# Optimization experiments

Hardware: AMD Instinct MI355X
Metric: run time of the kernel (lower is better)

## Reference

```python
import jax, jax.numpy as jnp
import numpy as np

B, S, D, V = 512, 64, 128, 256
NH = 4                 # sLSTM heads
HD = D // NH           # 32
INNER = 2 * D          # mLSTM inner dim (proj_factor=2.0)
NHM = 4                # mLSTM heads
DHM = INNER // NHM     # 64
BS = 4                 # qkv_proj_blocksize
NB = INNER // BS       # 64 block-diagonal qkv blocks
K = 4                  # causal conv kernel
FF = D                 # gated FFN up dim (proj_factor=1.0)


def setup_inputs():
    key = jax.random.key(0)
    ks = iter(jax.random.split(key, 40))
    def rn(shape, scale=0.02):
        return jax.random.normal(next(ks), shape, dtype=jnp.float32) * scale
    return {
        "x": jax.random.randint(next(ks), (B, S), 0, V, dtype=jnp.int32),
        "embed": rn((V, D), 0.02),
        "s_ln1": jnp.ones((2, D), jnp.float32),
        "s_gates_w": rn((2, 4, NH, HD, HD), 0.08),   # i,f,z,o headwise input projections
        "s_rec": rn((2, 4, NH, HD, HD), 0.08),       # block-diagonal recurrent kernels
        "s_bias": rn((2, 4, NH, HD), 0.1),
        "s_gn": jnp.ones((2, D), jnp.float32),
        "s_ln2": jnp.ones((2, D), jnp.float32),
        "s_ff_up": rn((2, D, 2 * FF), 0.05),
        "s_ff_down": rn((2, FF, D), 0.05),
        "m_ln1": jnp.ones((2, D), jnp.float32),
        "m_up": rn((2, D, 2 * INNER), 0.05),
        "m_conv_w": rn((2, INNER, K), 0.1),
        "m_conv_b": jnp.zeros((2, INNER), jnp.float32),
        "m_qkv_w": rn((2, 3, NB, BS, BS), 0.2),
        "m_ig_w": rn((2, 3 * INNER, NHM), 0.02),
        "m_ig_b": jnp.zeros((2, NHM), jnp.float32),
        "m_fg_w": rn((2, 3 * INNER, NHM), 0.02),
        "m_fg_b": 3.0 * jnp.ones((2, NHM), jnp.float32),
        "m_skip": jnp.ones((2, INNER), jnp.float32),
        "m_onorm": jnp.ones((2, INNER), jnp.float32),
        "m_down": rn((2, INNER, D), 0.05),
        "m_ln2": jnp.ones((2, D), jnp.float32),
        "m_ff_up": rn((2, D, 2 * FF), 0.05),
        "m_ff_down": rn((2, FF, D), 0.05),
        "post_ln": jnp.ones((D,), jnp.float32),
        "head_w": rn((D, V), 0.05),
        "head_b": jnp.zeros((V,), jnp.float32),
    }


def _ln(x, w, eps=1e-5):
    mu = x.mean(-1, keepdims=True)
    var = x.var(-1, keepdims=True)
    return (x - mu) * jax.lax.rsqrt(var + eps) * w


def _mh_ln(xh, w, eps=1e-5):
    # xh: [B,S,nh,dh]; per-head layernorm (GroupNorm), weight-only affine
    mu = xh.mean(-1, keepdims=True)
    var = xh.var(-1, keepdims=True)
    y = (xh - mu) * jax.lax.rsqrt(var + eps)
    return y * w.reshape(xh.shape[-2], xh.shape[-1])


def _ffn(x, up, down):
    g, u = jnp.split(x @ up, 2, axis=-1)
    return (jax.nn.gelu(g) * u) @ down


def _slstm(x, gw, rw, bias, gn):
    # vanilla sLSTM: stabilized exp-gated scalar-memory recurrence, block-diag recurrent kernels
    Bq, Sq, Dq = x.shape
    xh = x.reshape(Bq, Sq, NH, HD)
    # precompute input contributions for all 4 gates: [S,B,4,NH,HD]
    gx = jnp.einsum('bsnd,gned->sbgne', xh, gw) + bias

    def step(carry, g):
        h, c, n, m = carry
        raw = g + jnp.einsum('bnd,gned->bgne', h, rw)
        i_r, f_r, z_r, o_r = raw[:, 0], raw[:, 1], raw[:, 2], raw[:, 3]
        logfplusm = m + jax.nn.log_sigmoid(f_r)
        m_new = jnp.maximum(i_r, logfplusm)
        i = jnp.exp(i_r - m_new)
        f = jnp.exp(logfplusm - m_new)
        c_new = f * c + i * jnp.tanh(z_r)
        n_new = f * n + i
        h_new = jax.nn.sigmoid(o_r) * c_new / n_new
        return (h_new, c_new, n_new, m_new), h_new

    z0 = jnp.zeros((Bq, NH, HD), x.dtype)
    _, ys = jax.lax.scan(step, (z0, z0, z0, z0), gx)
    y = jnp.transpose(ys, (1, 0, 2, 3))  # [B,S,NH,HD]
    return _mh_ln(y, gn).reshape(Bq, Sq, Dq)


def _mlstm(x, up, cw, cb, qkvw, igw, igb, fgw, fgb, skip, onw, down):
    # pre-up-projection mLSTM layer with parallel stabilized matrix-memory cell
    Bq, Sq, _ = x.shape
    xm, z = jnp.split(x @ up, 2, axis=-1)  # [B,S,INNER] each
    # causal depthwise conv + swish
    conv = jax.lax.conv_general_dilated(
        xm.transpose(0, 2, 1), cw[:, None, :],
        window_strides=(1,), padding=[(K - 1, 0)], feature_group_count=INNER)
    x_conv = jax.nn.silu(conv.transpose(0, 2, 1) + cb)

    def hw(t, w):  # block-diagonal (headwise) linear, w: [NB, out, in]
        th = t.reshape(Bq, Sq, NB, BS)
        return jnp.einsum('bsni,noi->bsno', th, w).reshape(Bq, Sq, INNER)

    q = hw(x_conv, qkvw[0])
    k = hw(x_conv, qkvw[1])
    v = hw(xm, qkvw[2])

    gate_in = jnp.concatenate([q, k, v], axis=-1)          # [B,S,3*INNER]
    ig = (gate_in @ igw + igb).transpose(0, 2, 1)          # [B,NHM,S]
    fg = (gate_in @ fgw + fgb).transpose(0, 2, 1)

    qh = q.reshape(Bq, Sq, NHM, DHM).transpose(0, 2, 1, 3)  # [B,NHM,S,DHM]
    kh = k.reshape(Bq, Sq, NHM, DHM).transpose(0, 2, 1, 3)
    vh = v.reshape(Bq, Sq, NHM, DHM).transpose(0, 2, 1, 3)

    log_f = jax.nn.log_sigmoid(fg)                          # [B,NHM,S]
    c = jnp.concatenate([jnp.zeros_like(log_f[..., :1]), jnp.cumsum(log_f, -1)], -1)
    mat = c[..., 1:, None] - c[..., None, 1:]               # (i,j): sum_{t=j+1..i} log f_t
    mask = jnp.tril(jnp.ones((Sq, Sq), bool))
    log_D = jnp.where(mask, mat, -jnp.inf) + ig[..., None, :]
    max_log_D = jnp.max(log_D, -1, keepdims=True)           # [B,NHM,S,1]
    Dm = jnp.exp(log_D - max_log_D)
    qk = jnp.einsum('bhid,bhjd->bhij', qh, kh) * (DHM ** -0.5)
    Cm = qk * Dm
    norm = jnp.maximum(jnp.abs(Cm.sum(-1, keepdims=True)), jnp.exp(-max_log_D))
    Cn = Cm / (norm + 1e-6)
    h = jnp.einsum('bhij,bhjd->bhid', Cn, vh).transpose(0, 2, 1, 3)  # [B,S,NHM,DHM]
    h = _mh_ln(h, onw).reshape(Bq, Sq, INNER)
    h = (h + skip * x_conv) * jax.nn.silu(z)
    return h @ down


def _forward(x, embed, s_ln1, s_gates_w, s_rec, s_bias, s_gn, s_ln2, s_ff_up, s_ff_down,
             m_ln1, m_up, m_conv_w, m_conv_b, m_qkv_w, m_ig_w, m_ig_b, m_fg_w, m_fg_b,
             m_skip, m_onorm, m_down, m_ln2, m_ff_up, m_ff_down, post_ln, head_w, head_b):
    h = embed[x]  # [B,S,D]
    for i in range(2):
        # sLSTM block (even positions 0, 2)
        h = h + _slstm(_ln(h, s_ln1[i]), s_gates_w[i], s_rec[i], s_bias[i], s_gn[i])
        h = h + _ffn(_ln(h, s_ln2[i]), s_ff_up[i], s_ff_down[i])
        # mLSTM block (odd positions 1, 3)
        h = h + _mlstm(_ln(h, m_ln1[i]), m_up[i], m_conv_w[i], m_conv_b[i], m_qkv_w[i],
                       m_ig_w[i], m_ig_b[i], m_fg_w[i], m_fg_b[i], m_skip[i], m_onorm[i], m_down[i])
        h = h + _ffn(_ln(h, m_ln2[i]), m_ff_up[i], m_ff_down[i])
    h = _ln(h, post_ln)
    return h @ head_w + head_b


def reference(x, embed, s_ln1, s_gates_w, s_rec, s_bias, s_gn, s_ln2, s_ff_up, s_ff_down,
              m_ln1, m_up, m_conv_w, m_conv_b, m_qkv_w, m_ig_w, m_ig_b, m_fg_w, m_fg_b,
              m_skip, m_onorm, m_down, m_ln2, m_ff_up, m_ff_down, post_ln, head_w, head_b):
    return _forward(x, embed, s_ln1, s_gates_w, s_rec, s_bias, s_gn, s_ln2, s_ff_up, s_ff_down,
                    m_ln1, m_up, m_conv_w, m_conv_b, m_qkv_w, m_ig_w, m_ig_b, m_fg_w, m_fg_b,
                    m_skip, m_onorm, m_down, m_ln2, m_ff_up, m_ff_down, post_ln, head_w, head_b)
```

## Files before the change

kernel.cpp:

```cpp
#include <hip/hip_runtime.h>
#include <math.h>


__device__ __forceinline__ float sigf(float x){ return 1.f/(1.f+__expf(-x)); }
__device__ __forceinline__ float siluf(float x){ return x/(1.f+__expf(-x)); }
__device__ __forceinline__ float logsigf(float x){ return fminf(x,0.f) - log1pf(__expf(-fabsf(x))); }
__device__ __forceinline__ float geluf(float x){
  return 0.5f*x*(1.f+tanhf(0.7978845608028654f*(x+0.044715f*x*x*x)));
}
__device__ __forceinline__ void sums4(float4 v, float& s, float& q){
  s += v.x+v.y+v.z+v.w;
  q += v.x*v.x+v.y*v.y+v.z*v.z+v.w*v.w;
}

__device__ __forceinline__ void ln_rows(const float* __restrict__ src, const float* __restrict__ lnw,
                                        float* __restrict__ dst, int dstride,
                                        float (*red)[8], float (*red2)[8], int t)
{
  int r = t >> 3, l8 = t & 7;
  const float4* s4 = (const float4*)(src + (size_t)r*128 + l8*16);
  float4 v0=s4[0], v1=s4[1], v2=s4[2], v3=s4[3];
  float su=0.f, sq=0.f;
  sums4(v0,su,sq); sums4(v1,su,sq); sums4(v2,su,sq); sums4(v3,su,sq);
  red[r][l8]=su; red2[r][l8]=sq;
  __syncthreads();
  float ts=0.f, tq=0.f;
  #pragma unroll
  for (int k=0;k<8;k++){ ts+=red[r][k]; tq+=red2[r][k]; }
  float mu = ts*(1.f/128.f);
  float var = tq*(1.f/128.f) - mu*mu;
  float iv = rsqrtf(var+1e-5f);
  int c0 = l8*16;
  float vv[16];
  *(float4*)&vv[0]=v0; *(float4*)&vv[4]=v1; *(float4*)&vv[8]=v2; *(float4*)&vv[12]=v3;
  #pragma unroll
  for (int q2=0;q2<16;q2++) dst[r*dstride + c0 + q2] = (vv[q2]-mu)*iv*lnw[c0+q2];
}

__global__ __launch_bounds__(256) void k_embed(const int* __restrict__ x, const float* __restrict__ embed,
                                               float* __restrict__ h)
{
  int idx4 = blockIdx.x*256 + threadIdx.x;
  int tok = idx4 >> 5;
  int c4  = idx4 & 31;
  int id = x[tok];
  reinterpret_cast<float4*>(h)[idx4] = reinterpret_cast<const float4*>(embed)[id*32 + c4];
}

__global__ __launch_bounds__(512) void k_prep(
    const float* __restrict__ qkvw,
    const float* __restrict__ igw,
    const float* __restrict__ fgw,
    float* __restrict__ wtab)
{
  int t = threadIdx.x;
  int l = t >> 8, c = t & 255;
  int nb = c >> 2, i = c & 3;
  const float* qk  = qkvw + l*3072;
  const float* igl = igw + l*3072;
  const float* fgl = fgw + l*3072;
  float igc[4]={0,0,0,0}, igm[4]={0,0,0,0}, fgc[4]={0,0,0,0}, fgm[4]={0,0,0,0};
  #pragma unroll
  for (int o=0;o<4;o++){
    float wq = qk[nb*16 + o*4 + i];
    float wk = qk[1024 + nb*16 + o*4 + i];
    float wv = qk[2048 + nb*16 + o*4 + i];
    int no = nb*4+o;
    #pragma unroll
    for (int m=0;m<4;m++){
      igc[m] += wq*igl[no*4+m] + wk*igl[(256+no)*4+m];
      igm[m] += wv*igl[(512+no)*4+m];
      fgc[m] += wq*fgl[no*4+m] + wk*fgl[(256+no)*4+m];
      fgm[m] += wv*fgl[(512+no)*4+m];
    }
  }
  float* dst = wtab + l*4096;
  #pragma unroll
  for (int m=0;m<4;m++){
    dst[(0*256+c)*4+m] = igc[m];
    dst[(1*256+c)*4+m] = igm[m];
    dst[(2*256+c)*4+m] = fgc[m];
    dst[(3*256+c)*4+m] = fgm[m];
  }
}

__global__ __launch_bounds__(512) void k_slstm(
    float* __restrict__ h, const float* __restrict__ lnw,
    const float* __restrict__ gw, const float* __restrict__ rw,
    const float* __restrict__ bias, const float* __restrict__ gn)
{
  __shared__ float xh[64][128];
  __shared__ float hb[128];
  __shared__ float raw[512];
  __shared__ float red[64][8];
  __shared__ float red2[64][8];
  __shared__ float mu_s[64][4];
  __shared__ float iv_s[64][4];

  int t = threadIdx.x;
  int b = blockIdx.x;
  float* hrow = h + (size_t)b*8192;

  ln_rows(hrow, lnw, &xh[0][0], 128, red, red2, t);
  __syncthreads();

  int g  = t >> 7;
  int nh = (t >> 5) & 3;
  int e  = t & 31;
  float wg[32], wr[32];
  {
    const float4* g4 = (const float4*)(gw + (((g*4+nh)*32+e)*32));
    const float4* r4 = (const float4*)(rw + (((g*4+nh)*32+e)*32));
    #pragma unroll
    for (int q=0;q<8;q++){
      float4 a=g4[q]; wg[4*q]=a.x; wg[4*q+1]=a.y; wg[4*q+2]=a.z; wg[4*q+3]=a.w;
      float4 c=r4[q]; wr[4*q]=c.x; wr[4*q+1]=c.y; wr[4*q+2]=c.z; wr[4*q+3]=c.w;
    }
  }
  float bs = bias[(g*4+nh)*32+e];
  float c_s=0.f, n_s=0.f, m_s=0.f;
  if (t<128) hb[t]=0.f;
  __syncthreads();

  for (int s=0;s<64;s++){
    const float4* xr = (const float4*)&xh[s][nh*32];
    const float4* hr = (const float4*)&hb[nh*32];
    float acc = bs;
    #pragma unroll
    for (int q=0;q<8;q++){
      float4 xv = xr[q]; float4 hv = hr[q];
      acc += xv.x*wg[4*q+0] + xv.y*wg[4*q+1] + xv.z*wg[4*q+2] + xv.w*wg[4*q+3];
      acc += hv.x*wr[4*q+0] + hv.y*wr[4*q+1] + hv.z*wr[4*q+2] + hv.w*wr[4*q+3];
    }
    raw[t] = acc;
    __syncthreads();
    if (t < 128){
      float i_r = raw[t], f_r = raw[128+t], z_r = raw[256+t], o_r = raw[384+t];
      float lf = m_s + logsigf(f_r);
      float mn = fmaxf(i_r, lf);
      float iv = __expf(i_r-mn), fv = __expf(lf-mn);
      c_s = fv*c_s + iv*tanhf(z_r);
      n_s = fv*n_s + iv;
      m_s = mn;
      float hn = sigf(o_r)*c_s/n_s;
      hb[t] = hn;
      xh[s][t] = hn;
    }
    __syncthreads();
  }

  if (t < 256){
    int s = t>>2, n = t&3;
    const float4* yr = (const float4*)&xh[s][n*32];
    float su=0.f, sq=0.f;
    #pragma unroll
    for (int q=0;q<8;q++){ float4 v = yr[q]; sums4(v,su,sq); }
    float mu = su*(1.f/32.f);
    float var = sq*(1.f/32.f) - mu*mu;
    mu_s[s][n]=mu; iv_s[s][n]=rsqrtf(var+1e-5f);
  }
  __syncthreads();
  #pragma unroll
  for (int rr=0; rr<16; rr++){
    int idx = t + 512*rr;
    int s = idx>>7, c = idx&127;
    float y = (xh[s][c] - mu_s[s][c>>5]) * iv_s[s][c>>5] * gn[c];
    hrow[idx] += y;
  }
}

__global__ __launch_bounds__(256) void k_ffn(
    float* __restrict__ h, const float* __restrict__ lnw,
    const float* __restrict__ up, const float* __restrict__ down)
{
  __shared__ float xln[32][132];
  __shared__ float hid[32][132];
  __shared__ float bws[2][16][256];
  __shared__ float red[32][8];
  __shared__ float red2[32][8];
  int t = threadIdx.x;
  size_t tok0 = (size_t)blockIdx.x * 32;

  ln_rows(h + tok0*128, lnw, &xln[0][0], 132, red, red2, t);
  __syncthreads();

  int r0 = (t >> 5) * 4;
  int c0 = (t & 31) * 4;

  {
    float4 regs[4];
    auto stage = [&](int kc){
      #pragma unroll
      for (int j=0;j<4;j++){
        int idx = t + 256*j;
        int row = idx >> 6, c4 = idx & 63;
        regs[j] = *(const float4*)(up + (size_t)(kc*16+row)*256 + c4*4);
      }
    };
    auto wrt = [&](int buf){
      #pragma unroll
      for (int j=0;j<4;j++){
        int idx = t + 256*j;
        int row = idx >> 6, c4 = idx & 63;
        *(float4*)&bws[buf][row][c4*4] = regs[j];
      }
    };
    stage(0); wrt(0);
    __syncthreads();
    float4 ag[4], au[4];
    #pragma unroll
    for (int i=0;i<4;i++){ ag[i]=make_float4(0,0,0,0); au[i]=make_float4(0,0,0,0); }
    for (int kc=0;kc<8;kc++){
      if (kc<7) stage(kc+1);
      int buf = kc & 1;
      #pragma unroll
      for (int k=0;k<16;k++){
        float4 wg = *(float4*)&bws[buf][k][c0];
        float4 wu = *(float4*)&bws[buf][k][c0+128];
        int kk = kc*16 + k;
        #pragma unroll
        for (int i=0;i<4;i++){
          float xv = xln[r0+i][kk];
          ag[i].x+=xv*wg.x; ag[i].y+=xv*wg.y; ag[i].z+=xv*wg.z; ag[i].w+=xv*wg.w;
          au[i].x+=xv*wu.x; au[i].y+=xv*wu.y; au[i].z+=xv*wu.z; au[i].w+=xv*wu.w;
        }
      }
      if (kc<7) wrt(buf^1);
      __syncthreads();
    }
    #pragma unroll
    for (int i=0;i<4;i++){
      hid[r0+i][c0+0] = geluf(ag[i].x)*au[i].x;
      hid[r0+i][c0+1] = geluf(ag[i].y)*au[i].y;
      hid[r0+i][c0+2] = geluf(ag[i].z)*au[i].z;
      hid[r0+i][c0+3] = geluf(ag[i].w)*au[i].w;
    }
  }
  __syncthreads();

  {
    float (*bw2)[16][128] = (float (*)[16][128])bws;
    float4 regs[2];
    auto stage = [&](int kc){
      #pragma unroll
      for (int j=0;j<2;j++){
        int idx = t + 256*j;
        int row = idx >> 5, c4 = idx & 31;
        regs[j] = *(const float4*)(down + (size_t)(kc*16+row)*128 + c4*4);
      }
    };
    auto wrt = [&](int buf){
      #pragma unroll
      for (int j=0;j<2;j++){
        int idx = t + 256*j;
        int row = idx >> 5, c4 = idx & 31;
        *(float4*)&bw2[buf][row][c4*4] = regs[j];
      }
    };
    stage(0); wrt(0);
    __syncthreads();
    float4 a2[4];
    #pragma unroll
    for (int i=0;i<4;i++) a2[i]=make_float4(0,0,0,0);
    for (int kc=0;kc<8;kc++){
      if (kc<7) stage(kc+1);
      int buf = kc & 1;
      #pragma unroll
      for (int k=0;k<16;k++){
        float4 wv = *(float4*)&bw2[buf][k][c0];
        int kk = kc*16 + k;
        #pragma unroll
        for (int i=0;i<4;i++){
          float xv = hid[r0+i][kk];
          a2[i].x+=xv*wv.x; a2[i].y+=xv*wv.y; a2[i].z+=xv*wv.z; a2[i].w+=xv*wv.w;
        }
      }
      if (kc<7) wrt(buf^1);
      __syncthreads();
    }
    #pragma unroll
    for (int i=0;i<4;i++){
      float* dstp = h + (tok0 + r0 + i)*128 + c0;
      float4 hv = *(float4*)dstp;
      hv.x += a2[i].x; hv.y += a2[i].y; hv.z += a2[i].z; hv.w += a2[i].w;
      *(float4*)dstp = hv;
    }
  }
}

__global__ __launch_bounds__(256) void k_up(
    const float* __restrict__ h, const float* __restrict__ lnw,
    const float* __restrict__ up, float* __restrict__ xm, float* __restrict__ z)
{
  __shared__ float xln[64][132];
  __shared__ float bw[2][32][128];
  __shared__ float red[64][4];
  __shared__ float red2[64][4];
  int t = threadIdx.x;
  int mt = blockIdx.x >> 2, nt = blockIdx.x & 3;
  size_t tok0 = (size_t)mt * 64;
  int n0 = nt * 128;

  {
    int r = t >> 2, l = t & 3;
    const float4* s4 = (const float4*)(h + (tok0 + (size_t)r)*128 + l*32);
    float4 v[8];
    float su=0.f, sq=0.f;
    #pragma unroll
    for (int q=0;q<8;q++){ v[q]=s4[q]; sums4(v[q],su,sq); }
    red[r][l]=su; red2[r][l]=sq;
    __syncthreads();
    float ts=red[r][0]+red[r][1]+red[r][2]+red[r][3];
    float tq=red2[r][0]+red2[r][1]+red2[r][2]+red2[r][3];
    float mu=ts*(1.f/128.f);
    float var=tq*(1.f/128.f)-mu*mu;
    float iv=rsqrtf(var+1e-5f);
    int cb=l*32;
    #pragma unroll
    for (int q=0;q<8;q++){
      xln[r][cb+q*4+0]=(v[q].x-mu)*iv*lnw[cb+q*4+0];
      xln[r][cb+q*4+1]=(v[q].y-mu)*iv*lnw[cb+q*4+1];
      xln[r][cb+q*4+2]=(v[q].z-mu)*iv*lnw[cb+q*4+2];
      xln[r][cb+q*4+3]=(v[q].w-mu)*iv*lnw[cb+q*4+3];
    }
  }

  float4 regs[4];
  auto stage = [&](int kc){
    #pragma unroll
    for (int j=0;j<4;j++){
      int idx = t + 256*j;
      int row = idx >> 5, c4 = idx & 31;
      regs[j] = *(const float4*)(up + (size_t)(kc*32+row)*512 + n0 + c4*4);
    }
  };
  auto wrt = [&](int buf){
    #pragma unroll
    for (int j=0;j<4;j++){
      int idx = t + 256*j;
      int row = idx >> 5, c4 = idx & 31;
      *(float4*)&bw[buf][row][c4*4] = regs[j];
    }
  };
  stage(0); wrt(0);
  __syncthreads();

  int r0 = (t >> 5) * 8;
  int c0 = (t & 31) * 4;
  float4 acc4[8];
  #pragma unroll
  for (int i=0;i<8;i++) acc4[i]=make_float4(0,0,0,0);

  for (int kc=0;kc<4;kc++){
    if (kc<3) stage(kc+1);
    int buf = kc & 1;
    #pragma unroll 8
    for (int k=0;k<32;k++){
      float4 wv = *(float4*)&bw[buf][k][c0];
      int kk = kc*32 + k;
      #pragma unroll
      for (int i=0;i<8;i++){
        float xv = xln[r0+i][kk];
        acc4[i].x += xv*wv.x; acc4[i].y += xv*wv.y; acc4[i].z += xv*wv.z; acc4[i].w += xv*wv.w;
      }
    }
    if (kc<3) wrt(buf^1);
    __syncthreads();
  }

  float* dst; int cbase;
  if (n0 < 256){ dst = xm; cbase = n0 + c0; }
  else         { dst = z;  cbase = n0 - 256 + c0; }
  #pragma unroll
  for (int i=0;i<8;i++)
    *(float4*)(dst + (tok0 + r0 + i)*256 + cbase) = acc4[i];
}

__global__ __launch_bounds__(256) void k_convgates(
    const float* __restrict__ xm, float* __restrict__ xc,
    const float* __restrict__ cw, const float* __restrict__ cb,
    const float* __restrict__ wtab,
    const float* __restrict__ igb, const float* __restrict__ fgb,
    float* __restrict__ ig, float* __restrict__ fg)
{
  int t = threadIdx.x;
  int b = blockIdx.x;
  int c4 = t & 63, sr = t >> 6;
  int c0 = c4*4;
  const float* src = xm + (size_t)b*16384;
  float* dstc = xc + (size_t)b*16384;

  float4 r0 = *(const float4*)(cw + (c0+0)*4);
  float4 r1 = *(const float4*)(cw + (c0+1)*4);
  float4 r2 = *(const float4*)(cw + (c0+2)*4);
  float4 r3 = *(const float4*)(cw + (c0+3)*4);
  float4 wk0 = make_float4(r0.x, r1.x, r2.x, r3.x);
  float4 wk1 = make_float4(r0.y, r1.y, r2.y, r3.y);
  float4 wk2 = make_float4(r0.z, r1.z, r2.z, r3.z);
  float4 wk3 = make_float4(r0.w, r1.w, r2.w, r3.w);
  float4 bias4 = *(const float4*)(cb + c0);

  float4 Wigc[4], Wigm[4], Wfgc[4], Wfgm[4];
  #pragma unroll
  for (int i=0;i<4;i++){
    Wigc[i] = *(const float4*)(wtab + (0*256+c0+i)*4);
    Wigm[i] = *(const float4*)(wtab + (1*256+c0+i)*4);
    Wfgc[i] = *(const float4*)(wtab + (2*256+c0+i)*4);
    Wfgm[i] = *(const float4*)(wtab + (3*256+c0+i)*4);
  }

  int s0 = sr*16;
  float4 w0 = make_float4(0,0,0,0), w1 = w0, w2 = w0;
  if (s0 >= 3){
    w0 = *(const float4*)(src + (size_t)(s0-3)*256 + c0);
    w1 = *(const float4*)(src + (size_t)(s0-2)*256 + c0);
    w2 = *(const float4*)(src + (size_t)(s0-1)*256 + c0);
  }

  for (int j=0;j<16;j++){
    int s = s0 + j;
    float4 w3 = *(const float4*)(src + (size_t)s*256 + c0);
    float4 a;
    a.x = bias4.x + w0.x*wk0.x + w1.x*wk1.x + w2.x*wk2.x + w3.x*wk3.x;
    a.y = bias4.y + w0.y*wk0.y + w1.y*wk1.y + w2.y*wk2.y + w3.y*wk3.y;
    a.z = bias4.z + w0.z*wk0.z + w1.z*wk1.z + w2.z*wk2.z + w3.z*wk3.z;
    a.w = bias4.w + w0.w*wk0.w + w1.w*wk1.w + w2.w*wk2.w + w3.w*wk3.w;
    a.x = siluf(a.x); a.y = siluf(a.y); a.z = siluf(a.z); a.w = siluf(a.w);
    *(float4*)(dstc + (size_t)s*256 + c0) = a;

    float pig[4] = {0.f,0.f,0.f,0.f};
    float pfg[4] = {0.f,0.f,0.f,0.f};
    const float xcv[4] = {a.x,a.y,a.z,a.w};
    const float xmv[4] = {w3.x,w3.y,w3.z,w3.w};
    #pragma unroll
    for (int i=0;i<4;i++){
      pig[0] += xcv[i]*Wigc[i].x + xmv[i]*Wigm[i].x;
      pig[1] += xcv[i]*Wigc[i].y + xmv[i]*Wigm[i].y;
      pig[2] += xcv[i]*Wigc[i].z + xmv[i]*Wigm[i].z;
      pig[3] += xcv[i]*Wigc[i].w + xmv[i]*Wigm[i].w;
      pfg[0] += xcv[i]*Wfgc[i].x + xmv[i]*Wfgm[i].x;
      pfg[1] += xcv[i]*Wfgc[i].y + xmv[i]*Wfgm[i].y;
      pfg[2] += xcv[i]*Wfgc[i].z + xmv[i]*Wfgm[i].z;
      pfg[3] += xcv[i]*Wfgc[i].w + xmv[i]*Wfgm[i].w;
    }
    #pragma unroll
    for (int off=32; off>=1; off>>=1){
      #pragma unroll
      for (int m=0;m<4;m++){
        pig[m] += __shfl_xor(pig[m], off, 64);
        pfg[m] += __shfl_xor(pfg[m], off, 64);
      }
    }
    if (c4 == 0){
      #pragma unroll
      for (int m=0;m<4;m++){
        ig[(size_t)b*256 + m*64 + s] = pig[m] + igb[m];
        fg[(size_t)b*256 + m*64 + s] = pfg[m] + fgb[m];
      }
    }
    w0=w1; w1=w2; w2=w3;
  }
}

__global__ __launch_bounds__(256) void k_attn(
    float* __restrict__ xm, const float* __restrict__ xc,
    const float* __restrict__ qkvw,
    const float* __restrict__ igp, const float* __restrict__ fgp,
    const float* __restrict__ onorm)
{
  __shared__ float qs[64][68];
  __shared__ float ksm[64][68];
  __shared__ float vsm[64][68];
  __shared__ float cnm[64][65];
  __shared__ float csum[65];
  __shared__ float pmax[64];
  __shared__ float igl[64];
  __shared__ float lfs[64];
  __shared__ float nrec[64];

  int t = threadIdx.x;
  int b = blockIdx.x >> 2, hh = blockIdx.x & 3;
  const float* xcb = xc + (size_t)b*16384 + hh*64;
  float* xmb = xm + (size_t)b*16384 + hh*64;

  if (t < 64){
    lfs[t] = logsigf(fgp[(size_t)b*256 + hh*64 + t]);
    igl[t] = igp[(size_t)b*256 + hh*64 + t];
  }
  __syncthreads();

  int lb = t & 15;
  int nb = hh*16 + lb;
  float4 wq[4], wk[4], wv[4];
  #pragma unroll
  for (int o=0;o<4;o++){
    wq[o] = *(const float4*)(qkvw + nb*16 + o*4);
    wk[o] = *(const float4*)(qkvw + 1024 + nb*16 + o*4);
    wv[o] = *(const float4*)(qkvw + 2048 + nb*16 + o*4);
  }

  if (t == 0){
    float cacc = 0.f, pm = -1e30f;
    csum[0] = 0.f;
    for (int s=0;s<64;s++){
      cacc += lfs[s];
      csum[s+1] = cacc;
      pm = fmaxf(pm, igl[s] - cacc);
      pmax[s] = pm;
    }
  }

  #pragma unroll
  for (int j=0;j<4;j++){
    int s = (t >> 4) + j*16;
    float4 x4 = *(const float4*)(xcb + (size_t)s*256 + lb*4);
    float4 m4 = *(const float4*)(xmb + (size_t)s*256 + lb*4);
    float4 qv, kv, vv;
    qv.x = wq[0].x*x4.x + wq[0].y*x4.y + wq[0].z*x4.z + wq[0].w*x4.w;
    qv.y = wq[1].x*x4.x + wq[1].y*x4.y + wq[1].z*x4.z + wq[1].w*x4.w;
    qv.z = wq[2].x*x4.x + wq[2].y*x4.y + wq[2].z*x4.z + wq[2].w*x4.w;
    qv.w = wq[3].x*x4.x + wq[3].y*x4.y + wq[3].z*x4.z + wq[3].w*x4.w;
    kv.x = wk[0].x*x4.x + wk[0].y*x4.y + wk[0].z*x4.z + wk[0].w*x4.w;
    kv.y = wk[1].x*x4.x + wk[1].y*x4.y + wk[1].z*x4.z + wk[1].w*x4.w;
    kv.z = wk[2].x*x4.x + wk[2].y*x4.y + wk[2].z*x4.z + wk[2].w*x4.w;
    kv.w = wk[3].x*x4.x + wk[3].y*x4.y + wk[3].z*x4.z + wk[3].w*x4.w;
    vv.x = wv[0].x*m4.x + wv[0].y*m4.y + wv[0].z*m4.z + wv[0].w*m4.w;
    vv.y = wv[1].x*m4.x + wv[1].y*m4.y + wv[1].z*m4.z + wv[1].w*m4.w;
    vv.z = wv[2].x*m4.x + wv[2].y*m4.y + wv[2].z*m4.z + wv[2].w*m4.w;
    vv.w = wv[3].x*m4.x + wv[3].y*m4.y + wv[3].z*m4.z + wv[3].w*m4.w;
    *(float4*)&qs[s][lb*4]  = qv;
    *(float4*)&ksm[s][lb*4] = kv;
    *(float4*)&vsm[s][lb*4] = vv;
  }
  __syncthreads();

  int i = t >> 2;
  int jq = t & 3;
  float mi = csum[i+1] + pmax[i];

  float4 ql[16];
  #pragma unroll
  for (int kk=0;kk<16;kk++) ql[kk] = *(float4*)&qs[i][kk*4];

  int iwmax = ((t & ~63) >> 2) + 15;
  float rs = 0.f;
  for (int jj=0; jq + jj*4 <= iwmax && jj < 16; jj++){
    int j = jq + jj*4;
    if (j <= i){
      const float4* ka = (const float4*)&ksm[j][0];
      float dp = 0.f;
      #pragma unroll
      for (int kk=0;kk<16;kk++){
        float4 a = ql[kk], c = ka[kk];
        dp += a.x*c.x + a.y*c.y + a.z*c.z + a.w*c.w;
      }
      float val = dp * 0.125f * __expf(csum[i+1] - csum[j+1] + igl[j] - mi);
      cnm[i][j] = val;
      rs += val;
    }
  }
  rs += __shfl_xor(rs, 1, 4);
  rs += __shfl_xor(rs, 2, 4);
  if (jq == 0){
    float nm = fmaxf(fabsf(rs), __expf(-mi));
    nrec[i] = 1.f/(nm + 1e-6f);
  }
  __syncthreads();

  int d0 = jq*16;
  float acc[16];
  #pragma unroll
  for (int q=0;q<16;q++) acc[q]=0.f;
  float nr = nrec[i];
  for (int j=0;j<=i;j++){
    float cwv = cnm[i][j] * nr;
    const float4* va = (const float4*)&vsm[j][d0];
    #pragma unroll
    for (int q=0;q<4;q++){
      float4 v4 = va[q];
      acc[q*4+0] += cwv*v4.x; acc[q*4+1] += cwv*v4.y; acc[q*4+2] += cwv*v4.z; acc[q*4+3] += cwv*v4.w;
    }
  }
  float su=0.f, sq=0.f;
  #pragma unroll
  for (int q=0;q<16;q++){ su += acc[q]; sq += acc[q]*acc[q]; }
  su += __shfl_xor(su,1,4); su += __shfl_xor(su,2,4);
  sq += __shfl_xor(sq,1,4); sq += __shfl_xor(sq,2,4);
  float mu = su*(1.f/64.f);
  float var = sq*(1.f/64.f) - mu*mu;
  float ivr = rsqrtf(var + 1e-5f);
  const float* onw = onorm + hh*64 + d0;
  #pragma unroll
  for (int q=0;q<4;q++){
    float4 o4;
    o4.x = (acc[q*4+0]-mu)*ivr*onw[q*4+0];
    o4.y = (acc[q*4+1]-mu)*ivr*onw[q*4+1];
    o4.z = (acc[q*4+2]-mu)*ivr*onw[q*4+2];
    o4.w = (acc[q*4+3]-mu)*ivr*onw[q*4+3];
    *(float4*)(xmb + (size_t)i*256 + d0 + q*4) = o4;
  }
}

__global__ __launch_bounds__(256) void k_comb_down(
    float* __restrict__ h, const float* __restrict__ hln,
    const float* __restrict__ xc, const float* __restrict__ z,
    const float* __restrict__ skip, const float* __restrict__ down)
{
  __shared__ float comb[32][260];
  __shared__ float bw[2][16][128];
  int t = threadIdx.x;
  size_t tok0 = (size_t)blockIdx.x*32;
  #pragma unroll
  for (int j=0;j<8;j++){
    int f4 = t + 256*j;
    int r = f4 >> 6, c4 = f4 & 63;
    size_t gi = (tok0 + r)*256 + c4*4;
    float4 a  = *(const float4*)(hln + gi);
    float4 xv = *(const float4*)(xc + gi);
    float4 zv = *(const float4*)(z + gi);
    float4 sk = *(const float4*)(skip + c4*4);
    float4 o;
    o.x = (a.x + sk.x*xv.x)*siluf(zv.x);
    o.y = (a.y + sk.y*xv.y)*siluf(zv.y);
    o.z = (a.z + sk.z*xv.z)*siluf(zv.z);
    o.w = (a.w + sk.w*xv.w)*siluf(zv.w);
    *(float4*)&comb[r][c4*4] = o;
  }

  float4 regs[2];
  auto stage = [&](int kc){
    #pragma unroll
    for (int j=0;j<2;j++){
      int idx = t + 256*j;
      int row = idx >> 5, c4 = idx & 31;
      regs[j] = *(const float4*)(down + (size_t)(kc*16+row)*128 + c4*4);
    }
  };
  auto wrt = [&](int buf){
    #pragma unroll
    for (int j=0;j<2;j++){
      int idx = t + 256*j;
      int row = idx >> 5, c4 = idx & 31;
      *(float4*)&bw[buf][row][c4*4] = regs[j];
    }
  };
  stage(0); wrt(0);
  __syncthreads();

  int r0 = (t >> 5) * 4;
  int c0 = (t & 31) * 4;
  float4 a2[4];
  #pragma unroll
  for (int i=0;i<4;i++) a2[i]=make_float4(0,0,0,0);
  for (int kc=0;kc<16;kc++){
    if (kc<15) stage(kc+1);
    int buf = kc & 1;
    #pragma unroll
    for (int k=0;k<16;k++){
      float4 wv = *(float4*)&bw[buf][k][c0];
      int kk = kc*16 + k;
      #pragma unroll
      for (int i=0;i<4;i++){
        float xv = comb[r0+i][kk];
        a2[i].x+=xv*wv.x; a2[i].y+=xv*wv.y; a2[i].z+=xv*wv.z; a2[i].w+=xv*wv.w;
      }
    }
    if (kc<15) wrt(buf^1);
    __syncthreads();
  }
  #pragma unroll
  for (int i=0;i<4;i++){
    float* dstp = h + (tok0 + r0 + i)*128 + c0;
    float4 hv = *(float4*)dstp;
    hv.x += a2[i].x; hv.y += a2[i].y; hv.z += a2[i].z; hv.w += a2[i].w;
    *(float4*)dstp = hv;
  }
}

__global__ __launch_bounds__(256) void k_head(
    const float* __restrict__ h, const float* __restrict__ lnw,
    const float* __restrict__ w, const float* __restrict__ bias2,
    float* __restrict__ out)
{
  __shared__ float xln[32][132];
  __shared__ float bws[2][16][256];
  __shared__ float red[32][8];
  __shared__ float red2[32][8];
  int t = threadIdx.x;
  size_t tok0 = (size_t)blockIdx.x * 32;

  ln_rows(h + tok0*128, lnw, &xln[0][0], 132, red, red2, t);
  __syncthreads();

  float4 regs[4];
  auto stage = [&](int kc){
    #pragma unroll
    for (int j=0;j<4;j++){
      int idx = t + 256*j;
      int row = idx >> 6, c4 = idx & 63;
      regs[j] = *(const float4*)(w + (size_t)(kc*16+row)*256 + c4*4);
    }
  };
  auto wrt = [&](int buf){
    #pragma unroll
    for (int j=0;j<4;j++){
      int idx = t + 256*j;
      int row = idx >> 6, c4 = idx & 63;
      *(float4*)&bws[buf][row][c4*4] = regs[j];
    }
  };
  stage(0); wrt(0);
  __syncthreads();

  int r0 = (t >> 5) * 4;
  int c0 = (t & 31) * 8;
  float4 a0[4], a1[4];
  #pragma unroll
  for (int i=0;i<4;i++){ a0[i]=make_float4(0,0,0,0); a1[i]=make_float4(0,0,0,0); }
  for (int kc=0;kc<8;kc++){
    if (kc<7) stage(kc+1);
    int buf = kc & 1;
    #pragma unroll
    for (int k=0;k<16;k++){
      float4 w0 = *(float4*)&bws[buf][k][c0];
      float4 w1 = *(float4*)&bws[buf][k][c0+4];
      int kk = kc*16 + k;
      #pragma unroll
      for (int i=0;i<4;i++){
        float xv = xln[r0+i][kk];
        a0[i].x+=xv*w0.x; a0[i].y+=xv*w0.y; a0[i].z+=xv*w0.z; a0[i].w+=xv*w0.w;
        a1[i].x+=xv*w1.x; a1[i].y+=xv*w1.y; a1[i].z+=xv*w1.z; a1[i].w+=xv*w1.w;
      }
    }
    if (kc<7) wrt(buf^1);
    __syncthreads();
  }
  float4 b0 = *(const float4*)(bias2 + c0);
  float4 b1 = *(const float4*)(bias2 + c0 + 4);
  #pragma unroll
  for (int i=0;i<4;i++){
    float* dstp = out + (tok0 + r0 + i)*256 + c0;
    float4 o0, o1;
    o0.x=a0[i].x+b0.x; o0.y=a0[i].y+b0.y; o0.z=a0[i].z+b0.z; o0.w=a0[i].w+b0.w;
    o1.x=a1[i].x+b1.x; o1.y=a1[i].y+b1.y; o1.z=a1[i].z+b1.z; o1.w=a1[i].w+b1.w;
    ((float4*)dstp)[0]=o0; ((float4*)dstp)[1]=o1;
  }
}

extern "C" void kernel_launch(void* const* d_in, const int* in_sizes, int n_in,
                              void* d_out, int out_size, void* d_ws, size_t ws_size,
                              hipStream_t stream)
{
  const int*   x      = (const int*)  d_in[0];
  const float* embed  = (const float*)d_in[1];
  const float* s_ln1  = (const float*)d_in[2];
  const float* s_gw   = (const float*)d_in[3];
  const float* s_rec  = (const float*)d_in[4];
  const float* s_bias = (const float*)d_in[5];
  const float* s_gn   = (const float*)d_in[6];
  const float* s_ln2  = (const float*)d_in[7];
  const float* s_ffu  = (const float*)d_in[8];
  const float* s_ffd  = (const float*)d_in[9];
  const float* m_ln1  = (const float*)d_in[10];
  const float* m_up   = (const float*)d_in[11];
  const float* m_cw   = (const float*)d_in[12];
  const float* m_cb   = (const float*)d_in[13];
  const float* m_qkv  = (const float*)d_in[14];
  const float* m_igw  = (const float*)d_in[15];
  const float* m_igb  = (const float*)d_in[16];
  const float* m_fgw  = (const float*)d_in[17];
  const float* m_fgb  = (const float*)d_in[18];
  const float* m_skip = (const float*)d_in[19];
  const float* m_onw  = (const float*)d_in[20];
  const float* m_down = (const float*)d_in[21];
  const float* m_ln2  = (const float*)d_in[22];
  const float* m_ffu  = (const float*)d_in[23];
  const float* m_ffd  = (const float*)d_in[24];
  const float* postln = (const float*)d_in[25];
  const float* headw  = (const float*)d_in[26];
  const float* headb  = (const float*)d_in[27];

  float* p = (float*)d_ws;
  float* hbuf = p; p += 4194304;
  size_t avail = ws_size / 4;
  const size_t need_full = 4194304ULL + 3ULL*8388608ULL + 2ULL*131072ULL + 8192ULL;
  float* xmbuf;
  if (avail >= need_full){ xmbuf = p; p += 8388608; }
  else                   { xmbuf = (float*)d_out; }
  float* zbuf  = p; p += 8388608;
  float* xcbuf = p; p += 8388608;
  float* igbuf = p; p += 131072;
  float* fgbuf = p; p += 131072;
  float* wtab  = p; p += 8192;

  k_prep<<<1, 512, 0, stream>>>(m_qkv, m_igw, m_fgw, wtab);
  k_embed<<<4096, 256, 0, stream>>>(x, embed, hbuf);

  for (int i=0;i<2;i++){
    k_slstm<<<512, 512, 0, stream>>>(hbuf, s_ln1+i*128, s_gw+i*16384, s_rec+i*16384,
                                     s_bias+i*512, s_gn+i*128);
    k_ffn<<<1024, 256, 0, stream>>>(hbuf, s_ln2+i*128, s_ffu+i*32768, s_ffd+i*16384);
    k_up<<<2048, 256, 0, stream>>>(hbuf, m_ln1+i*128, m_up+i*65536, xmbuf, zbuf);
    k_convgates<<<512, 256, 0, stream>>>(xmbuf, xcbuf, m_cw+i*1024, m_cb+i*256,
                                         wtab+i*4096, m_igb+i*4, m_fgb+i*4,
                                         igbuf, fgbuf);
    k_attn<<<2048, 256, 0, stream>>>(xmbuf, xcbuf, m_qkv+i*3072, igbuf, fgbuf, m_onw+i*256);
    k_comb_down<<<1024, 256, 0, stream>>>(hbuf, xmbuf, xcbuf, zbuf, m_skip+i*256, m_down+i*32768);
    k_ffn<<<1024, 256, 0, stream>>>(hbuf, m_ln2+i*128, m_ffu+i*32768, m_ffd+i*16384);
  }

  k_head<<<1024, 256, 0, stream>>>(hbuf, postln, headw, headb, (float*)d_out);
}
```

Baseline: 1.167 ms.

## Split sLSTM into separate layernorm kernel and per-head single-wavefront scan

Moves the input layernorm into its own kernel writing to a scratch buffer, then runs the sLSTM recurrence with one 64-thread block per (batch, head), giving 2048 blocks instead of 512. Each lane computes two gate pre-activations and exchanges them across half-waves with shuffles, so all 64 lanes evaluate the cell update redundantly instead of staging raw gates through shared memory. The goal is more parallelism and shorter per-step work on the serial recurrence, which is latency-bound. The costs are an extra kernel launch, a global round-trip for the normalized input, and 128 weight registers per lane, which may limit occupancy.

```diff
diff --git a/kernel.cpp b/kernel.cpp
--- a/kernel.cpp
+++ b/kernel.cpp
@@ -84,88 +84,115 @@
   }
 }
 
-__global__ __launch_bounds__(512) void k_slstm(
-    float* __restrict__ h, const float* __restrict__ lnw,
+__global__ __launch_bounds__(256) void k_lnx(
+    const float* __restrict__ h, const float* __restrict__ lnw, float* __restrict__ dst)
+{
+  __shared__ float red[32][8];
+  __shared__ float red2[32][8];
+  size_t tok0 = (size_t)blockIdx.x * 32;
+  ln_rows(h + tok0*128, lnw, dst + tok0*128, 128, red, red2, threadIdx.x);
+}
+
+__global__ __launch_bounds__(64, 2) void k_sscan(
+    float* __restrict__ h, const float* __restrict__ xls,
     const float* __restrict__ gw, const float* __restrict__ rw,
     const float* __restrict__ bias, const float* __restrict__ gn)
 {
-  __shared__ float xh[64][128];
-  __shared__ float hb[128];
-  __shared__ float raw[512];
-  __shared__ float red[64][8];
-  __shared__ float red2[64][8];
-  __shared__ float mu_s[64][4];
-  __shared__ float iv_s[64][4];
-
-  int t = threadIdx.x;
-  int b = blockIdx.x;
-  float* hrow = h + (size_t)b*8192;
-
-  ln_rows(hrow, lnw, &xh[0][0], 128, red, red2, t);
-  __syncthreads();
-
-  int g  = t >> 7;
-  int nh = (t >> 5) & 3;
-  int e  = t & 31;
-  float wg[32], wr[32];
+  __shared__ float xs[64][36];
+  __shared__ float hb[32];
+  __shared__ float ys[64][36];
+
+  int l = threadIdx.x;
+  int b = blockIdx.x >> 2, nh = blockIdx.x & 3;
+  const float* xbase = xls + (size_t)b*8192 + nh*32;
+
+  #pragma unroll
+  for (int it=0; it<8; it++){
+    int u = l + 64*it;
+    int r = u >> 3, c4 = u & 7;
+    float4 v = *(const float4*)(xbase + (size_t)r*128 + c4*4);
+    *(float4*)&xs[r][c4*4] = v;
+  }
+
+  int g0 = (l >> 5) * 2;
+  int e  = l & 31;
+  float wg0[32], wg1[32], wr0[32], wr1[32];
   {
-    const float4* g4 = (const float4*)(gw + (((g*4+nh)*32+e)*32));
-    const float4* r4 = (const float4*)(rw + (((g*4+nh)*32+e)*32));
+    const float4* a = (const float4*)(gw + (((g0  )*4+nh)*32+e)*32);
+    const float4* bq= (const float4*)(gw + (((g0+1)*4+nh)*32+e)*32);
+    const float4* c = (const float4*)(rw + (((g0  )*4+nh)*32+e)*32);
+    const float4* d = (const float4*)(rw + (((g0+1)*4+nh)*32+e)*32);
     #pragma unroll
     for (int q=0;q<8;q++){
-      float4 a=g4[q]; wg[4*q]=a.x; wg[4*q+1]=a.y; wg[4*q+2]=a.z; wg[4*q+3]=a.w;
-      float4 c=r4[q]; wr[4*q]=c.x; wr[4*q+1]=c.y; wr[4*q+2]=c.z; wr[4*q+3]=c.w;
-    }
-  }
-  float bs = bias[(g*4+nh)*32+e];
+      float4 va=a[q]; wg0[4*q]=va.x; wg0[4*q+1]=va.y; wg0[4*q+2]=va.z; wg0[4*q+3]=va.w;
+      float4 vb=bq[q];wg1[4*q]=vb.x; wg1[4*q+1]=vb.y; wg1[4*q+2]=vb.z; wg1[4*q+3]=vb.w;
+      float4 vc=c[q]; wr0[4*q]=vc.x; wr0[4*q+1]=vc.y; wr0[4*q+2]=vc.z; wr0[4*q+3]=vc.w;
+      float4 vd=d[q]; wr1[4*q]=vd.x; wr1[4*q+1]=vd.y; wr1[4*q+2]=vd.z; wr1[4*q+3]=vd.w;
+    }
+  }
+  float bs0 = bias[((g0  )*4+nh)*32+e];
+  float bs1 = bias[((g0+1)*4+nh)*32+e];
+
+  if (l < 32) hb[l] = 0.f;
   float c_s=0.f, n_s=0.f, m_s=0.f;
-  if (t<128) hb[t]=0.f;
   __syncthreads();
 
   for (int s=0;s<64;s++){
-    const float4* xr = (const float4*)&xh[s][nh*32];
-    const float4* hr = (const float4*)&hb[nh*32];
-    float acc = bs;
+    float acc0 = bs0, acc1 = bs1;
+    const float4* xr = (const float4*)&xs[s][0];
+    const float4* hr = (const float4*)&hb[0];
     #pragma unroll
     for (int q=0;q<8;q++){
       float4 xv = xr[q]; float4 hv = hr[q];
-      acc += xv.x*wg[4*q+0] + xv.y*wg[4*q+1] + xv.z*wg[4*q+2] + xv.w*wg[4*q+3];
-      acc += hv.x*wr[4*q+0] + hv.y*wr[4*q+1] + hv.z*wr[4*q+2] + hv.w*wr[4*q+3];
-    }
-    raw[t] = acc;
+      acc0 += xv.x*wg0[4*q+0] + xv.y*wg0[4*q+1] + xv.z*wg0[4*q+2] + xv.w*wg0[4*q+3];
+      acc0 += hv.x*wr0[4*q+0] + hv.y*wr0[4*q+1] + hv.z*wr0[4*q+2] + hv.w*wr0[4*q+3];
+      acc1 += xv.x*wg1[4*q+0] + xv.y*wg1[4*q+1] + xv.z*wg1[4*q+2] + xv.w*wg1[4*q+3];
+      acc1 += hv.x*wr1[4*q+0] + hv.y*wr1[4*q+1] + hv.z*wr1[4*q+2] + hv.w*wr1[4*q+3];
+    }
+    float othr0 = __shfl_xor(acc0, 32, 64);
+    float othr1 = __shfl_xor(acc1, 32, 64);
+    bool lo = (l < 32);
+    float i_r = lo ? acc0 : othr0;
+    float f_r = lo ? acc1 : othr1;
+    float z_r = lo ? othr0 : acc0;
+    float o_r = lo ? othr1 : acc1;
+
+    float lf = m_s + logsigf(f_r);
+    float mn = fmaxf(i_r, lf);
+    float iv = __expf(i_r-mn), fv = __expf(lf-mn);
+    c_s = fv*c_s + iv*tanhf(z_r);
+    n_s = fv*n_s + iv;
+    m_s = mn;
+    float hn = sigf(o_r)*c_s/n_s;
     __syncthreads();
-    if (t < 128){
-      float i_r = raw[t], f_r = raw[128+t], z_r = raw[256+t], o_r = raw[384+t];
-      float lf = m_s + logsigf(f_r);
-      float mn = fmaxf(i_r, lf);
-      float iv = __expf(i_r-mn), fv = __expf(lf-mn);
-      c_s = fv*c_s + iv*tanhf(z_r);
-      n_s = fv*n_s + iv;
-      m_s = mn;
-      float hn = sigf(o_r)*c_s/n_s;
-      hb[t] = hn;
-      xh[s][t] = hn;
-    }
+    if (lo){ hb[e] = hn; ys[s][e] = hn; }
     __syncthreads();
   }
 
-  if (t < 256){
-    int s = t>>2, n = t&3;
-    const float4* yr = (const float4*)&xh[s][n*32];
+  {
+    float v[32];
     float su=0.f, sq=0.f;
-    #pragma unroll
-    for (int q=0;q<8;q++){ float4 v = yr[q]; sums4(v,su,sq); }
+    const float4* yr = (const float4*)&ys[l][0];
+    #pragma unroll
+    for (int q=0;q<8;q++){
+      float4 y4 = yr[q];
+      v[4*q]=y4.x; v[4*q+1]=y4.y; v[4*q+2]=y4.z; v[4*q+3]=y4.w;
+      sums4(y4, su, sq);
+    }
     float mu = su*(1.f/32.f);
     float var = sq*(1.f/32.f) - mu*mu;
-    mu_s[s][n]=mu; iv_s[s][n]=rsqrtf(var+1e-5f);
-  }
-  __syncthreads();
-  #pragma unroll
-  for (int rr=0; rr<16; rr++){
-    int idx = t + 512*rr;
-    int s = idx>>7, c = idx&127;
-    float y = (xh[s][c] - mu_s[s][c>>5]) * iv_s[s][c>>5] * gn[c];
-    hrow[idx] += y;
+    float ivr = rsqrtf(var+1e-5f);
+    float* dst = h + ((size_t)b*64 + l)*128 + nh*32;
+    const float* gnh = gn + nh*32;
+    #pragma unroll
+    for (int q=0;q<8;q++){
+      float4 hv = *(float4*)(dst + q*4);
+      hv.x += (v[4*q+0]-mu)*ivr*gnh[4*q+0];
+      hv.y += (v[4*q+1]-mu)*ivr*gnh[4*q+1];
+      hv.z += (v[4*q+2]-mu)*ivr*gnh[4*q+2];
+      hv.w += (v[4*q+3]-mu)*ivr*gnh[4*q+3];
+      *(float4*)(dst + q*4) = hv;
+    }
   }
 }
 
@@ -797,7 +824,8 @@
   k_embed<<<4096, 256, 0, stream>>>(x, embed, hbuf);
 
   for (int i=0;i<2;i++){
-    k_slstm<<<512, 512, 0, stream>>>(hbuf, s_ln1+i*128, s_gw+i*16384, s_rec+i*16384,
+    k_lnx<<<1024, 256, 0, stream>>>(hbuf, s_ln1+i*128, xcbuf);
+    k_sscan<<<2048, 64, 0, stream>>>(hbuf, xcbuf, s_gw+i*16384, s_rec+i*16384,
                                      s_bias+i*512, s_gn+i*128);
     k_ffn<<<1024, 256, 0, stream>>>(hbuf, s_ln2+i*128, s_ffu+i*32768, s_ffd+i*16384);
     k_up<<<2048, 256, 0, stream>>>(hbuf, m_ln1+i*128, m_up+i*65536, xmbuf, zbuf);
```

Result: slower. 1.212 ms (+3.9%).
